# Performance work log

Measured on AMD Instinct MI355X. Metric: run time of the kernel, lower is better.

## Reference

```python
import jax, jax.numpy as jnp
import numpy as np

B, S, E, FFN, Q = 8, 2048, 512, 2048, 8


def setup_inputs() -> dict:
    key = jax.random.key(0)
    k0, k1, k2, k3 = jax.random.split(key, 4)
    x = jax.random.normal(k0, (B, S, E), dtype=jnp.float32)
    ry = jax.random.normal(k1, (Q,), dtype=jnp.float32)  # trainable RY angles
    w1 = jax.random.normal(k2, (FFN, Q), dtype=jnp.float32) / np.sqrt(Q).astype(np.float32)
    b1 = jnp.zeros((FFN,), dtype=jnp.float32)
    w2 = jax.random.normal(k3, (E, FFN), dtype=jnp.float32) / np.sqrt(FFN).astype(np.float32)
    b2 = jnp.zeros((E,), dtype=jnp.float32)
    return {"x": x, "ry": ry, "w1": w1, "b1": b1, "w2": w2, "b2": b2}


def reference(x, ry, w1, b1, w2, b2):
    # Quantum layer: each qubit i starts in |0>, gets RX(x[..., i]) then RY(ry[i]),
    # then PauliZ expectation. Product state => closed form <Z_i> = cos(x_i) * cos(ry_i).
    nq = ry.shape[0]
    z = jnp.cos(x[..., :nq]) * jnp.cos(ry)  # [B, S, Q]
    # dropout is identity in eval mode
    h = jnp.einsum("bsq,fq->bsf", z, w1) + b1  # fc1
    return jnp.einsum("bsf,ef->bse", jax.nn.relu(h), w2) + b2  # fc2
```

## Files before the change

### kernel.cpp

```cpp
#include <hip/hip_runtime.h>
#include <cstdint>
#include <cstddef>


typedef __attribute__((ext_vector_type(8))) short s16x8;
typedef __attribute__((ext_vector_type(4))) float f32x4;

__device__ __forceinline__ unsigned short f2bf(float f) {
  unsigned int u = __float_as_uint(f);
  unsigned int r = u + 0x7fffu + ((u >> 16) & 1u);
  return (unsigned short)(r >> 16);
}

__device__ __forceinline__ void async_copy16(const void* g, void* l) {
  __builtin_amdgcn_global_load_lds(
      (const __attribute__((address_space(1))) void*)(uintptr_t)g,
      (__attribute__((address_space(3))) void*)(unsigned int)(uintptr_t)l,
      16, 0, 0);
}

__global__ __launch_bounds__(256) void k_w2(const float* __restrict__ w2,
                                            unsigned short* __restrict__ img) {
  const int n = blockIdx.x;
  const int t = threadIdx.x;
  const int s = t >> 2, quad = t & 3;
  const float* src = w2 + (size_t)n * 2048 + t * 8;
  float4 a = *(const float4*)src;
  float4 b = *(const float4*)(src + 4);
  uint4 pk;
  pk.x = f2bf(a.x) | ((unsigned)f2bf(a.y) << 16);
  pk.y = f2bf(a.z) | ((unsigned)f2bf(a.w) << 16);
  pk.z = f2bf(b.x) | ((unsigned)f2bf(b.y) << 16);
  pk.w = f2bf(b.z) | ((unsigned)f2bf(b.w) << 16);
  const int nt = n >> 8, nl = n & 255, nhi = nl >> 4, nlo = nl & 15;
  const size_t ci = (size_t)(nt * 64 + s) * 1024 + nhi * 64 + quad * 16 + nlo;
  *(uint4*)(img + ci * 8) = pk;
}

__global__ __launch_bounds__(256, 2) void k_fused(
    const float* __restrict__ x, const float* __restrict__ ry,
    const float* __restrict__ w1, const float* __restrict__ b1,
    const unsigned short* __restrict__ w2b, const float* __restrict__ b2,
    float* __restrict__ C) {
  __shared__ unsigned short As[2][64 * 32];
  __shared__ float b1s[2048];

  const int t = threadIdx.x;
  const int lane = t & 63;
  const int w = t >> 6;
  const int mt = (int)(blockIdx.x >> 1);
  const int nt = (int)(blockIdx.x & 1);
  const int r0 = mt * 64;
  const int c0 = nt * 256;
  const int fp = t & 15;
  const int rq = t >> 4;
  const int fr = lane & 15;
  const int quad = lane >> 4;

  float zr[4][8];
  {
    float4 ra = *(const float4*)ry;
    float4 rb = *(const float4*)(ry + 4);
    float cy[8] = {__cosf(ra.x), __cosf(ra.y), __cosf(ra.z), __cosf(ra.w),
                   __cosf(rb.x), __cosf(rb.y), __cosf(rb.z), __cosf(rb.w)};
#pragma unroll
    for (int r = 0; r < 4; ++r) {
      const float* xr = x + (size_t)(r0 + rq * 4 + r) * 512;
      float4 x0 = *(const float4*)xr;
      float4 x1 = *(const float4*)(xr + 4);
      zr[r][0] = __cosf(x0.x) * cy[0];
      zr[r][1] = __cosf(x0.y) * cy[1];
      zr[r][2] = __cosf(x0.z) * cy[2];
      zr[r][3] = __cosf(x0.w) * cy[3];
      zr[r][4] = __cosf(x1.x) * cy[4];
      zr[r][5] = __cosf(x1.y) * cy[5];
      zr[r][6] = __cosf(x1.z) * cy[6];
      zr[r][7] = __cosf(x1.w) * cy[7];
    }
  }
  __builtin_amdgcn_sched_barrier(0);

  const char* gBb =
      (const char*)w2b +
      ((size_t)nt * 64 * 1024 + (size_t)w * 256 + quad * 16 + fr) * 16;
#define LOADB(S, D)                                        \
  {                                                        \
    const char* p_ = gBb + (size_t)(S) * 16384;            \
    D[0] = *(const s16x8*)(p_);                            \
    D[1] = *(const s16x8*)(p_ + 1024);                     \
    D[2] = *(const s16x8*)(p_ + 2048);                     \
    D[3] = *(const s16x8*)(p_ + 3072);                     \
  }

  async_copy16(b1 + (size_t)t * 4, (char*)b1s + (size_t)t * 16);
  async_copy16(b1 + (size_t)(t + 256) * 4, (char*)b1s + (size_t)(t + 256) * 16);
  s16x8 Bp[4], Bq[4];
  LOADB(0, Bp);
  f32x4 wA0, wA1, wA2, wA3, wB0, wB1, wB2, wB3;
  {
    const f32x4* p0 = (const f32x4*)(w1 + fp * 16);
    wA0 = p0[0]; wA1 = p0[1]; wA2 = p0[2]; wA3 = p0[3];
    const f32x4* p1 = (const f32x4*)(w1 + 256 + fp * 16);
    wB0 = p1[0]; wB1 = p1[1]; wB2 = p1[2]; wB3 = p1[3];
  }
  asm volatile("s_waitcnt vmcnt(0) lgkmcnt(0)" ::: "memory");
  __builtin_amdgcn_sched_barrier(0);
  __builtin_amdgcn_s_barrier();

  const int q0 = rq & 1;
  const int koct = fp >> 2, fpl = fp & 3;
  const int sA_off = ((koct ^ ((rq * 2) & 3)) << 4) + fpl * 4;
  const int sB_off = ((koct ^ ((rq * 2 + 1) & 3)) << 4) + fpl * 4;
  const int rw0 = ((rq * 4 + 0) ^ q0) * 64;
  const int rw1 = ((rq * 4 + 1) ^ q0) * 64;
  const int rw2 = ((rq * 4 + 2) ^ q0) * 64;
  const int rw3 = ((rq * 4 + 3) ^ q0) * 64;

  auto act = [&](int s, int buf, const f32x4& v0, const f32x4& v1,
                 const f32x4& v2, const f32x4& v3) {
    const float bb0 = b1s[s * 32 + fp * 2];
    const float bb1 = b1s[s * 32 + fp * 2 + 1];
    unsigned int u0, u1, u2, u3;
#define ACT_ROW(R, UD)                                                      \
  {                                                                         \
    float h0 = bb0, h1 = bb1;                                               \
    h0 += zr[R][0] * v0[0]; h1 += zr[R][0] * v2[0];                         \
    h0 += zr[R][1] * v0[1]; h1 += zr[R][1] * v2[1];                         \
    h0 += zr[R][2] * v0[2]; h1 += zr[R][2] * v2[2];                         \
    h0 += zr[R][3] * v0[3]; h1 += zr[R][3] * v2[3];                         \
    h0 += zr[R][4] * v1[0]; h1 += zr[R][4] * v3[0];                         \
    h0 += zr[R][5] * v1[1]; h1 += zr[R][5] * v3[1];                         \
    h0 += zr[R][6] * v1[2]; h1 += zr[R][6] * v3[2];                         \
    h0 += zr[R][7] * v1[3]; h1 += zr[R][7] * v3[3];                         \
    h0 = fmaxf(h0, 0.0f);                                                   \
    h1 = fmaxf(h1, 0.0f);                                                   \
    asm("v_cvt_pk_bf16_f32 %0, %1, %2" : "=v"(UD) : "v"(h0), "v"(h1));      \
  }
    ACT_ROW(0, u0) ACT_ROW(1, u1) ACT_ROW(2, u2) ACT_ROW(3, u3)
#undef ACT_ROW
    char* base = (char*)As + buf * 4096;
    *(unsigned int*)(base + rw0 + sA_off) = q0 ? u1 : u0;
    *(unsigned int*)(base + rw1 + sA_off) = q0 ? u0 : u1;
    *(unsigned int*)(base + rw2 + sB_off) = q0 ? u3 : u2;
    *(unsigned int*)(base + rw3 + sB_off) = q0 ? u2 : u3;
  };

  act(0, 0, wA0, wA1, wA2, wA3);
  asm volatile("s_waitcnt lgkmcnt(0)" ::: "memory");
  __builtin_amdgcn_sched_barrier(0);
  __builtin_amdgcn_s_barrier();

  const int wn = w * 64;
  const char* pAb =
      (const char*)As + fr * 64 + ((quad ^ ((fr >> 1) & 3)) << 4);

  f32x4 acc[4][4];
#pragma unroll
  for (int i = 0; i < 4; ++i)
#pragma unroll
    for (int j = 0; j < 4; ++j) acc[i][j] = (f32x4){0.f, 0.f, 0.f, 0.f};

#define BODY(KT, BU, BL, WU0, WU1, WU2, WU3, WL0, WL1, WL2, WL3, BPRE,      \
             WPRE, ACTG, VMC)                                               \
  {                                                                         \
    if (BPRE) LOADB((KT) + 1, BL);                                          \
    if (WPRE) {                                                             \
      const f32x4* wp =                                                     \
          (const f32x4*)(w1 + (size_t)((KT) + 2) * 256 + fp * 16);          \
      WL0 = wp[0]; WL1 = wp[1]; WL2 = wp[2]; WL3 = wp[3];                   \
    }                                                                       \
    asm volatile("s_waitcnt vmcnt(" VMC ")" ::: "memory");                  \
    __builtin_amdgcn_sched_barrier(0);                                      \
    s16x8 af[4];                                                            \
    {                                                                       \
      const char* pA = pAb + ((KT) & 1) * 4096;                             \
      af[0] = *(const s16x8*)(pA);                                          \
      af[1] = *(const s16x8*)(pA + 1024);                                   \
      af[2] = *(const s16x8*)(pA + 2048);                                   \
      af[3] = *(const s16x8*)(pA + 3072);                                   \
    }                                                                       \
    if (ACTG) act((KT) + 1, ((KT) + 1) & 1, WU0, WU1, WU2, WU3);            \
    asm volatile("s_waitcnt lgkmcnt(0)" ::: "memory");                      \
    __builtin_amdgcn_sched_barrier(0);                                      \
    __builtin_amdgcn_s_setprio(1);                                          \
    _Pragma("unroll") for (int i = 0; i < 4; ++i)                           \
        _Pragma("unroll") for (int j = 0; j < 4; ++j) acc[i][j] =           \
        __builtin_amdgcn_mfma_f32_16x16x32_bf16(af[i], BU[j], acc[i][j],    \
                                                0, 0, 0);                   \
    __builtin_amdgcn_s_setprio(0);                                          \
    __builtin_amdgcn_s_barrier();                                           \
  }

  for (int kt = 0; kt < 62; kt += 2) {
    BODY(kt, Bp, Bq, wB0, wB1, wB2, wB3, wA0, wA1, wA2, wA3, true, true,
         true, "8");
    BODY(kt + 1, Bq, Bp, wA0, wA1, wA2, wA3, wB0, wB1, wB2, wB3, true, true,
         true, "8");
  }
  BODY(62, Bp, Bq, wB0, wB1, wB2, wB3, wA0, wA1, wA2, wA3, true, false, true,
       "4");
  BODY(63, Bq, Bp, wA0, wA1, wA2, wA3, wB0, wB1, wB2, wB3, false, false,
       false, "0");
#undef BODY
#undef LOADB

  float bias[4];
#pragma unroll
  for (int j = 0; j < 4; ++j) bias[j] = b2[c0 + wn + j * 16 + fr];
#pragma unroll
  for (int i = 0; i < 4; ++i) {
    const int rbase = r0 + i * 16 + quad * 4;
#pragma unroll
    for (int rr = 0; rr < 4; ++rr) {
      float* crow = C + (size_t)(rbase + rr) * 512;
#pragma unroll
      for (int j = 0; j < 4; ++j)
        crow[c0 + wn + j * 16 + fr] = acc[i][j][rr] + bias[j];
    }
  }
}

__global__ __launch_bounds__(256) void k_naive(
    const float* __restrict__ x, const float* __restrict__ ry,
    const float* __restrict__ w1, const float* __restrict__ b1,
    const float* __restrict__ w2, const float* __restrict__ b2,
    float* __restrict__ out) {
  __shared__ float zsh[8];
  __shared__ float acts[2048];
  const int r = blockIdx.x;
  const int t = threadIdx.x;
  if (t < 8) zsh[t] = __cosf(x[(size_t)r * 512 + t]) * __cosf(ry[t]);
  __syncthreads();
  float z[8];
#pragma unroll
  for (int q = 0; q < 8; ++q) z[q] = zsh[q];
#pragma unroll
  for (int i = 0; i < 8; ++i) {
    const int f = t * 8 + i;
    const float* wr = w1 + (size_t)f * 8;
    float4 a = *(const float4*)wr;
    float4 b = *(const float4*)(wr + 4);
    float h = b1[f] + z[0] * a.x + z[1] * a.y + z[2] * a.z + z[3] * a.w +
              z[4] * b.x + z[5] * b.y + z[6] * b.z + z[7] * b.w;
    acts[f] = fmaxf(h, 0.0f);
  }
  __syncthreads();
  for (int ee = 0; ee < 2; ++ee) {
    const int e = t + ee * 256;
    const float* wr = w2 + (size_t)e * 2048;
    float acc = b2[e];
    for (int f = 0; f < 2048; f += 4) {
      float4 wv = *(const float4*)(wr + f);
      float4 av = *(const float4*)(acts + f);
      acc += av.x * wv.x + av.y * wv.y + av.z * wv.z + av.w * wv.w;
    }
    out[(size_t)r * 512 + e] = acc;
  }
}

extern "C" void kernel_launch(void* const* d_in, const int* in_sizes, int n_in,
                              void* d_out, int out_size, void* d_ws,
                              size_t ws_size, hipStream_t stream) {
  const float* x  = (const float*)d_in[0];
  const float* ry = (const float*)d_in[1];
  const float* w1 = (const float*)d_in[2];
  const float* b1 = (const float*)d_in[3];
  const float* w2 = (const float*)d_in[4];
  const float* b2 = (const float*)d_in[5];
  float* out = (float*)d_out;

  const size_t w2b_bytes = (size_t)512 * 2048 * 2;
  if (ws_size < w2b_bytes) {
    k_naive<<<dim3(16384), dim3(256), 0, stream>>>(x, ry, w1, b1, w2, b2, out);
    return;
  }
  unsigned short* w2b = (unsigned short*)d_ws;
  k_w2<<<dim3(512), dim3(256), 0, stream>>>(w2, w2b);
  k_fused<<<dim3(512), dim3(256), 0, stream>>>(x, ry, w1, b1, w2b, b2, out);
}
```

Baseline: 138.8 us.

## Split FFN reduction dimension across two wave groups with LDS reduction

Doubles the block to 512 threads and splits the 2048-wide hidden (K) dimension between two groups of four waves. Each group computes its own activations and MFMA partial sums over half of K. The partials are then combined through a shared-memory reduction before the bias add and store. This halves the serial K loop per block and adds more waves per CU to hide latency. In exchange it costs extra LDS (16 KB reduction buffer plus duplicated A tiles), extra barriers, and higher register pressure at 512 threads with a launch bound of 2 blocks.

```diff
diff --git a/kernel.cpp b/kernel.cpp
--- a/kernel.cpp
+++ b/kernel.cpp
@@ -37,23 +37,27 @@
   *(uint4*)(img + ci * 8) = pk;
 }
 
-__global__ __launch_bounds__(256, 2) void k_fused(
+__global__ __launch_bounds__(512, 2) void k_fused(
     const float* __restrict__ x, const float* __restrict__ ry,
     const float* __restrict__ w1, const float* __restrict__ b1,
     const unsigned short* __restrict__ w2b, const float* __restrict__ b2,
     float* __restrict__ C) {
-  __shared__ unsigned short As[2][64 * 32];
+  __shared__ unsigned short As[2][2][64 * 32];
   __shared__ float b1s[2048];
+  __shared__ f32x4 red[1024];
 
   const int t = threadIdx.x;
   const int lane = t & 63;
   const int w = t >> 6;
+  const int ks = w >> 2;
+  const int wl = w & 3;
+  const int tg = t & 255;
   const int mt = (int)(blockIdx.x >> 1);
   const int nt = (int)(blockIdx.x & 1);
   const int r0 = mt * 64;
   const int c0 = nt * 256;
-  const int fp = t & 15;
-  const int rq = t >> 4;
+  const int fp = tg & 15;
+  const int rq = tg >> 4;
   const int fr = lane & 15;
   const int quad = lane >> 4;
 
@@ -82,25 +86,27 @@
 
   const char* gBb =
       (const char*)w2b +
-      ((size_t)nt * 64 * 1024 + (size_t)w * 256 + quad * 16 + fr) * 16;
-#define LOADB(S, D)                                        \
-  {                                                        \
-    const char* p_ = gBb + (size_t)(S) * 16384;            \
-    D[0] = *(const s16x8*)(p_);                            \
-    D[1] = *(const s16x8*)(p_ + 1024);                     \
-    D[2] = *(const s16x8*)(p_ + 2048);                     \
-    D[3] = *(const s16x8*)(p_ + 3072);                     \
+      (((size_t)nt * 64 + (size_t)ks * 32) * 1024 + (size_t)wl * 256 +
+       (size_t)quad * 16 + fr) * 16;
+  const float* w1g = w1 + (size_t)ks * 8192;
+  const float* b1g = b1s + (size_t)ks * 1024;
+#define LOADB(S, D)                                \
+  {                                                \
+    const char* p_ = gBb + (size_t)(S) * 16384;    \
+    D[0] = *(const s16x8*)(p_);                    \
+    D[1] = *(const s16x8*)(p_ + 1024);             \
+    D[2] = *(const s16x8*)(p_ + 2048);             \
+    D[3] = *(const s16x8*)(p_ + 3072);             \
   }
 
   async_copy16(b1 + (size_t)t * 4, (char*)b1s + (size_t)t * 16);
-  async_copy16(b1 + (size_t)(t + 256) * 4, (char*)b1s + (size_t)(t + 256) * 16);
   s16x8 Bp[4], Bq[4];
   LOADB(0, Bp);
   f32x4 wA0, wA1, wA2, wA3, wB0, wB1, wB2, wB3;
   {
-    const f32x4* p0 = (const f32x4*)(w1 + fp * 16);
+    const f32x4* p0 = (const f32x4*)(w1g + fp * 16);
     wA0 = p0[0]; wA1 = p0[1]; wA2 = p0[2]; wA3 = p0[3];
-    const f32x4* p1 = (const f32x4*)(w1 + 256 + fp * 16);
+    const f32x4* p1 = (const f32x4*)(w1g + 256 + fp * 16);
     wB0 = p1[0]; wB1 = p1[1]; wB2 = p1[2]; wB3 = p1[3];
   }
   asm volatile("s_waitcnt vmcnt(0) lgkmcnt(0)" ::: "memory");
@@ -115,11 +121,12 @@
   const int rw1 = ((rq * 4 + 1) ^ q0) * 64;
   const int rw2 = ((rq * 4 + 2) ^ q0) * 64;
   const int rw3 = ((rq * 4 + 3) ^ q0) * 64;
+  char* asg = (char*)As + (size_t)ks * 8192;
 
   auto act = [&](int s, int buf, const f32x4& v0, const f32x4& v1,
                  const f32x4& v2, const f32x4& v3) {
-    const float bb0 = b1s[s * 32 + fp * 2];
-    const float bb1 = b1s[s * 32 + fp * 2 + 1];
+    const float bb0 = b1g[s * 32 + fp * 2];
+    const float bb1 = b1g[s * 32 + fp * 2 + 1];
     unsigned int u0, u1, u2, u3;
 #define ACT_ROW(R, UD)                                                      \
   {                                                                         \
@@ -138,7 +145,7 @@
   }
     ACT_ROW(0, u0) ACT_ROW(1, u1) ACT_ROW(2, u2) ACT_ROW(3, u3)
 #undef ACT_ROW
-    char* base = (char*)As + buf * 4096;
+    char* base = asg + buf * 4096;
     *(unsigned int*)(base + rw0 + sA_off) = q0 ? u1 : u0;
     *(unsigned int*)(base + rw1 + sA_off) = q0 ? u0 : u1;
     *(unsigned int*)(base + rw2 + sB_off) = q0 ? u3 : u2;
@@ -150,9 +157,8 @@
   __builtin_amdgcn_sched_barrier(0);
   __builtin_amdgcn_s_barrier();
 
-  const int wn = w * 64;
-  const char* pAb =
-      (const char*)As + fr * 64 + ((quad ^ ((fr >> 1) & 3)) << 4);
+  const int wn = wl * 64;
+  const char* pAb = asg + fr * 64 + ((quad ^ ((fr >> 1) & 3)) << 4);
 
   f32x4 acc[4][4];
 #pragma unroll
@@ -166,7 +172,7 @@
     if (BPRE) LOADB((KT) + 1, BL);                                          \
     if (WPRE) {                                                             \
       const f32x4* wp =                                                     \
-          (const f32x4*)(w1 + (size_t)((KT) + 2) * 256 + fp * 16);          \
+          (const f32x4*)(w1g + (size_t)((KT) + 2) * 256 + fp * 16);         \
       WL0 = wp[0]; WL1 = wp[1]; WL2 = wp[2]; WL3 = wp[3];                   \
     }                                                                       \
     asm volatile("s_waitcnt vmcnt(" VMC ")" ::: "memory");                  \
@@ -191,31 +197,51 @@
     __builtin_amdgcn_s_barrier();                                           \
   }
 
-  for (int kt = 0; kt < 62; kt += 2) {
+  for (int kt = 0; kt < 30; kt += 2) {
     BODY(kt, Bp, Bq, wB0, wB1, wB2, wB3, wA0, wA1, wA2, wA3, true, true,
          true, "8");
     BODY(kt + 1, Bq, Bp, wA0, wA1, wA2, wA3, wB0, wB1, wB2, wB3, true, true,
          true, "8");
   }
-  BODY(62, Bp, Bq, wB0, wB1, wB2, wB3, wA0, wA1, wA2, wA3, true, false, true,
-       "4");
-  BODY(63, Bq, Bp, wA0, wA1, wA2, wA3, wB0, wB1, wB2, wB3, false, false,
+  BODY(30, Bp, Bq, wB0, wB1, wB2, wB3, wA0, wA1, wA2, wA3, true, false, true,
+       "8");
+  BODY(31, Bq, Bp, wA0, wA1, wA2, wA3, wB0, wB1, wB2, wB3, false, false,
        false, "0");
 #undef BODY
 #undef LOADB
 
-  float bias[4];
-#pragma unroll
-  for (int j = 0; j < 4; ++j) bias[j] = b2[c0 + wn + j * 16 + fr];
 #pragma unroll
   for (int i = 0; i < 4; ++i) {
-    const int rbase = r0 + i * 16 + quad * 4;
-#pragma unroll
-    for (int rr = 0; rr < 4; ++rr) {
-      float* crow = C + (size_t)(rbase + rr) * 512;
-#pragma unroll
-      for (int j = 0; j < 4; ++j)
-        crow[c0 + wn + j * 16 + fr] = acc[i][j][rr] + bias[j];
+    if (ks) {
+      red[tg * 4 + 0] = acc[i][0];
+      red[tg * 4 + 1] = acc[i][1];
+      red[tg * 4 + 2] = acc[i][2];
+      red[tg * 4 + 3] = acc[i][3];
+    }
+    __syncthreads();
+    if (!ks) {
+      acc[i][0] += red[tg * 4 + 0];
+      acc[i][1] += red[tg * 4 + 1];
+      acc[i][2] += red[tg * 4 + 2];
+      acc[i][3] += red[tg * 4 + 3];
+    }
+    __syncthreads();
+  }
+
+  if (ks == 0) {
+    float bias[4];
+#pragma unroll
+    for (int j = 0; j < 4; ++j) bias[j] = b2[c0 + wn + j * 16 + fr];
+#pragma unroll
+    for (int i = 0; i < 4; ++i) {
+      const int rbase = r0 + i * 16 + quad * 4;
+#pragma unroll
+      for (int rr = 0; rr < 4; ++rr) {
+        float* crow = C + (size_t)(rbase + rr) * 512;
+#pragma unroll
+        for (int j = 0; j < 4; ++j)
+          crow[c0 + wn + j * 16 + fr] = acc[i][j][rr] + bias[j];
+      }
     }
   }
 }
@@ -276,5 +302,5 @@
   }
   unsigned short* w2b = (unsigned short*)d_ws;
   k_w2<<<dim3(512), dim3(256), 0, stream>>>(w2, w2b);
-  k_fused<<<dim3(512), dim3(256), 0, stream>>>(x, ry, w1, b1, w2b, b2, out);
-}
+  k_fused<<<dim3(512), dim3(512), 0, stream>>>(x, ry, w1, b1, w2b, b2, out);
+}
```

New measurement: 149.4 us. 7.6% more time.
